# Kernel optimization log

Hardware: AMD Instinct MI355X
Metric: run time of the kernel (lower is better)

## Reference

```python
import jax, jax.numpy as jnp
import numpy as np

EPS = 1e-5
LAMB = 1.0
N_VARS = 40000
N_EDGES = 200000
N_CONF = 100000
FEAT = 128
DOM = 4
T_MAX = 3


def setup_inputs() -> dict:
    key = jax.random.key(0)
    ks = jax.random.split(key, 16)
    # initial node states: torch.rand then row-normalized (F.normalize dim=1)
    s = jax.random.uniform(ks[0], (N_VARS, FEAT), dtype=jnp.float32)
    state0 = s / jnp.maximum(jnp.linalg.norm(s, axis=1, keepdims=True), 1e-12)
    def lin(k, fan_in, shape):
        return jax.random.normal(k, shape, dtype=jnp.float32) / np.sqrt(fan_in)
    inp = {
        'state0': state0,
        'W1': lin(ks[1], 2 * FEAT, (2 * FEAT, FEAT)),
        'b1': jnp.zeros((FEAT,), jnp.float32),
        'W2': lin(ks[2], FEAT, (FEAT, FEAT)),
        'b2': jnp.zeros((FEAT,), jnp.float32),
        'ln_g': jnp.ones((FEAT,), jnp.float32),
        'ln_b': jnp.zeros((FEAT,), jnp.float32),
        'bn_g': jnp.ones((FEAT,), jnp.float32),
        'bn_b': jnp.zeros((FEAT,), jnp.float32),
        'Wd': lin(ks[3], FEAT, (FEAT, DOM)),
        'bd': jnp.zeros((DOM,), jnp.float32),
        # positive relation/confidence matrices so -log(...) is finite
        'relation': jax.random.uniform(ks[4], (DOM, DOM), jnp.float32, 0.1, 1.0),
        'confidence_mat': jax.random.uniform(ks[5], (DOM, DOM), jnp.float32, 0.1, 1.0),
        # positive degrees (divisor)
        'degrees': jax.random.uniform(ks[6], (N_VARS,), jnp.float32, 1.0, 33.0),
        'idx_left': jax.random.randint(ks[7], (N_EDGES,), 0, N_VARS, jnp.int32),
        'idx_right': jax.random.randint(ks[8], (N_EDGES,), 0, N_VARS, jnp.int32),
        'idx_left_pos': jax.random.randint(ks[9], (N_CONF,), 0, N_VARS, jnp.int32),
        'idx_right_pos': jax.random.randint(ks[10], (N_CONF,), 0, N_VARS, jnp.int32),
        'iterations': T_MAX,
    }
    return inp


def reference(state0, W1, b1, W2, b2, ln_g, ln_b, bn_g, bn_b, Wd, bd,
              relation, confidence_mat, degrees,
              idx_left, idx_right, idx_left_pos, idx_right_pos, iterations):
    N, F = state0.shape
    E = idx_left.shape[0]
    degs = degrees[:, None]

    def mlp(x):  # Linear-ReLU-Linear-ReLU-LayerNorm
        h = jax.nn.relu(x @ W1 + b1)
        h = jax.nn.relu(h @ W2 + b2)
        mu = jnp.mean(h, axis=-1, keepdims=True)
        var = jnp.var(h, axis=-1, keepdims=True)  # biased, like torch LayerNorm
        return ln_g * (h - mu) * jax.lax.rsqrt(var + EPS) + ln_b

    state = state0
    logits_list = []
    for _ in range(iterations):
        xl = state[idx_left]          # [E, F] gather
        xr = state[idx_right]
        # mpnn(in_right=xl, in_left=xr): in_lr = cat(xr, xl); in_rl = cat(xl, xr)
        msg = jnp.concatenate([jnp.concatenate([xr, xl], axis=1),
                               jnp.concatenate([xl, xr], axis=1)], axis=0)  # [2E, 2F]
        h = mlp(msg)
        agg = (jnp.zeros((N, F), state.dtype)
               .at[idx_left].add(h[:E])
               .at[idx_right].add(h[E:]))  # scatter-add messages
        rec = agg / degs
        # BatchNorm1d, training mode (batch stats over nodes)
        mu = jnp.mean(rec, axis=0)
        var = jnp.var(rec, axis=0)
        state = bn_g * (rec - mu) * jax.lax.rsqrt(var + EPS) + bn_b
        logits_list.append(state @ Wd + bd)

    phi = jax.nn.softmax(jnp.stack(logits_list, axis=1), axis=2)  # [N, T, D]
    T, D = phi.shape[1], phi.shape[2]
    all_phi = phi.reshape(N, T * D)

    def pair_loss(mat, il, ir, denom):
        pl = all_phi[il].reshape(-1, D)   # [E*T, D]
        pr = all_phi[ir].reshape(-1, D)
        s = jnp.sum((pl @ mat) * pr, axis=1)
        return jnp.sum(-jnp.log(s)) / denom

    n_conflicts = jnp.float32(E)
    n_confidence = jnp.float32(idx_left_pos.shape[0])
    loss = (pair_loss(relation, idx_left, idx_right, n_conflicts)
            + LAMB * pair_loss(confidence_mat, idx_left_pos, idx_right_pos, 10.0 * n_confidence))

    assignment = jnp.argmax(phi, axis=2).astype(jnp.int32)  # [N, T]
    valid = relation[assignment[idx_left], assignment[idx_right]]  # [E, T]
    edge_conflicts = 1.0 - valid
    n_conf = jnp.sum(edge_conflicts[:, -1])
    conflict_ratio = n_conf / n_conflicts
    return (loss, conflict_ratio, phi, edge_conflicts, assignment[:, -1], n_conf)
```

## Files before the change

### kernel.cpp

```cpp
#include <hip/hip_runtime.h>
#include <math.h>

#define N_VARS 40000
#define FEAT 128
#define N_EDGES 200000
#define N_MSG (2*N_EDGES)
#define N_CONFP 100000
#define T_ITERS 3
#define EPSF 1e-5f

#define NB_CONF 782
#define NB_PAIR 1172
#define NB_STAT 157
#define NB_STAT2 625
#define NB_MSG64 6250
#define OUT_TOTAL 1120003
#define NCONF_SLOT 1120002

typedef short short8 __attribute__((ext_vector_type(8)));
typedef float floatx4 __attribute__((ext_vector_type(4)));
typedef unsigned short ushort4v __attribute__((ext_vector_type(4)));
typedef unsigned uint4v __attribute__((ext_vector_type(4)));

__device__ __forceinline__ float scrub0(float x){
  unsigned u = __float_as_uint(x);
  return ((u & 0x7F800000u) == 0x7F800000u) ? 0.f : x;
}
__device__ __forceinline__ unsigned short f2bf_rne(float x){
  unsigned u = __float_as_uint(x);
  u += 0x7FFFu + ((u >> 16) & 1u);
  return (unsigned short)(u >> 16);
}
__device__ __forceinline__ float bf2f(unsigned short h){
  return __uint_as_float(((unsigned)h) << 16);
}
__device__ __forceinline__ unsigned cvtpk(float lo, float hi){
  unsigned r;
  asm("v_cvt_pk_bf16_f32 %0, %1, %2" : "=v"(r) : "v"(lo), "v"(hi));
  return r;
}

__global__ __launch_bounds__(256) void k_zero_int(int* __restrict__ p, int n){
  int i = blockIdx.x*256 + threadIdx.x;
  if (i < n) p[i] = 0;
}

__global__ __launch_bounds__(256) void k_hist(const int* __restrict__ idxL,
    const int* __restrict__ idxR, int* __restrict__ cnt){
  int m = blockIdx.x*256 + threadIdx.x;
  if (m < N_MSG){
    int t = (m < N_EDGES) ? idxL[m] : idxR[m - N_EDGES];
    atomicAdd(&cnt[t], 1);
  }
}
__global__ __launch_bounds__(256) void k_scan1(const int* __restrict__ cnt,
    int* __restrict__ pos, int* __restrict__ blk_tot){
  const int tid = threadIdx.x;
  const int idx = blockIdx.x*256 + tid;
  int v = (idx < N_VARS) ? cnt[idx] : 0;
  __shared__ int sh[256];
  sh[tid] = v;
  __syncthreads();
#pragma unroll
  for (int o = 1; o < 256; o <<= 1){
    int add = (tid >= o) ? sh[tid - o] : 0;
    __syncthreads();
    sh[tid] += add;
    __syncthreads();
  }
  if (idx < N_VARS) pos[idx] = sh[tid] - v;
  if (tid == 255) blk_tot[blockIdx.x] = sh[255];
}
__global__ __launch_bounds__(256) void k_scan2(const int* __restrict__ blk_tot,
    int* __restrict__ blk_off){
  const int tid = threadIdx.x;
  int v = (tid < NB_STAT) ? blk_tot[tid] : 0;
  __shared__ int sh[256];
  sh[tid] = v;
  __syncthreads();
#pragma unroll
  for (int o = 1; o < 256; o <<= 1){
    int add = (tid >= o) ? sh[tid - o] : 0;
    __syncthreads();
    sh[tid] += add;
    __syncthreads();
  }
  if (tid < NB_STAT) blk_off[tid] = sh[tid] - v;
}
__global__ __launch_bounds__(256) void k_scan3(int* __restrict__ pos,
    const int* __restrict__ blk_off){
  const int idx = blockIdx.x*256 + threadIdx.x;
  if (idx < N_VARS) pos[idx] += blk_off[blockIdx.x];
}
__global__ __launch_bounds__(256) void k_fill(const int* __restrict__ idxL,
    const int* __restrict__ idxR, int* __restrict__ pos,
    int2* __restrict__ pairs){
  int m = blockIdx.x*256 + threadIdx.x;
  if (m < N_MSG){
    int e = (m < N_EDGES) ? m : (m - N_EDGES);
    int l = idxL[e], r = idxR[e];
    int t = (m < N_EDGES) ? l : r;
    int o = (m < N_EDGES) ? r : l;
    int slot = atomicAdd(&pos[t], 1);
    pairs[slot] = make_int2(t, o);
  }
}

__global__ __launch_bounds__(256) void k_prep2(const float* __restrict__ W2,
                                               const float* __restrict__ W1,
                                               unsigned short* __restrict__ W2pack,
                                               unsigned short* __restrict__ W1pack){
  if (blockIdx.x < 8){
    int gid = blockIdx.x*256 + threadIdx.x;
    int lane = gid & 63;
    int ks = (gid >> 6) & 3;
    int ntg = gid >> 8;
    int kbase = ks*32 + (lane >> 4)*8;
    int n = ntg*16 + (lane & 15);
#pragma unroll
    for (int j = 0; j < 8; ++j)
      W2pack[gid*8 + j] = f2bf_rne(W2[(kbase + j)*FEAT + n]);
  } else {
    int gid = (blockIdx.x - 8)*256 + threadIdx.x;
    int lane = gid & 63;
    int ks = (gid >> 6) & 3;
    int ntg = gid >> 8;
    int kbase = ks*32 + (lane >> 4)*8;
    int n = ntg*16 + (lane & 15);
#pragma unroll
    for (int j = 0; j < 8; ++j){
      int k = kbase + j;
      float v = (n < 128) ? W1[k*FEAT + n] : W1[(128 + k)*FEAT + (n - 128)];
      W1pack[gid*8 + j] = f2bf_rne(v);
    }
  }
}

#define X_STRIDE 136
__global__ __launch_bounds__(256) void k_pq(const float* __restrict__ xf,
                                            const unsigned short* __restrict__ xb,
                                            int src_f32,
                                            const unsigned short* __restrict__ W1pack,
                                            const float* __restrict__ b1v,
                                            unsigned short* __restrict__ PQb,
                                            float* __restrict__ red,
                                            float4* __restrict__ recz){
  __shared__ __align__(16) unsigned short Xbf[32*X_STRIDE];
  const int tid = threadIdx.x;
  const int row0 = blockIdx.x * 32;
  if (blockIdx.x == 0) red[tid] = 0.f;
  {
    const int zid = blockIdx.x*256 + tid;
#pragma unroll
    for (int i = 0; i < 4; ++i)
      recz[zid + i*320000] = make_float4(0.f,0.f,0.f,0.f);
  }
  if (src_f32){
    const int c4 = (tid & 31)*4, g8 = tid >> 5;
#pragma unroll
    for (int r = 0; r < 4; ++r){
      int row = g8*4 + r;
      const float4 v = *(const float4*)&xf[(row0 + row)*FEAT + c4];
      uint2 uu;
      uu.x = cvtpk(v.x, v.y);
      uu.y = cvtpk(v.z, v.w);
      *(uint2*)&Xbf[row*X_STRIDE + c4] = uu;
    }
  } else {
    const int c8 = (tid & 15)*8, g16 = tid >> 4;
#pragma unroll
    for (int r = 0; r < 2; ++r){
      int row = r*16 + g16;
      *(short8*)&Xbf[row*X_STRIDE + c8] = *(const short8*)&xb[(row0 + row)*FEAT + c8];
    }
  }
  __syncthreads();
  const int w = tid >> 6, lane = tid & 63;
  const int quad = lane >> 4, mcol = lane & 15;
  float bi0 = 0.f, bi1 = 0.f, bi2 = 0.f, bi3 = 0.f;
  if (w >= 2){
    int nb = (w - 2)*64 + mcol;
    bi0 = b1v[nb]; bi1 = b1v[nb + 16]; bi2 = b1v[nb + 32]; bi3 = b1v[nb + 48];
  }
#pragma unroll
  for (int mt = 0; mt < 2; ++mt){
    floatx4 a0 = {bi0,bi0,bi0,bi0};
    floatx4 a1 = {bi1,bi1,bi1,bi1};
    floatx4 a2 = {bi2,bi2,bi2,bi2};
    floatx4 a3 = {bi3,bi3,bi3,bi3};
#pragma unroll
    for (int ks = 0; ks < 4; ++ks){
      short8 a = *(const short8*)&Xbf[(mt*16 + mcol)*X_STRIDE + ks*32 + quad*8];
      const unsigned short* bp = W1pack + ((w*16 + ks)*64 + lane)*8;
      short8 b0 = *(const short8*)(bp);
      short8 b1 = *(const short8*)(bp + 2048);
      short8 b2 = *(const short8*)(bp + 4096);
      short8 b3 = *(const short8*)(bp + 6144);
      a0 = __builtin_amdgcn_mfma_f32_16x16x32_bf16(a, b0, a0, 0, 0, 0);
      a1 = __builtin_amdgcn_mfma_f32_16x16x32_bf16(a, b1, a1, 0, 0, 0);
      a2 = __builtin_amdgcn_mfma_f32_16x16x32_bf16(a, b2, a2, 0, 0, 0);
      a3 = __builtin_amdgcn_mfma_f32_16x16x32_bf16(a, b3, a3, 0, 0, 0);
    }
#pragma unroll
    for (int reg = 0; reg < 4; ++reg){
      unsigned u01 = cvtpk(a0[reg], a1[reg]);
      unsigned u23 = cvtpk(a2[reg], a3[reg]);
      size_t base = (size_t)(row0 + mt*16 + quad*4 + reg)*(2*FEAT) + w*64 + mcol;
      PQb[base]      = (unsigned short)u01;
      PQb[base + 16] = (unsigned short)(u01 >> 16);
      PQb[base + 32] = (unsigned short)u23;
      PQb[base + 48] = (unsigned short)(u23 >> 16);
    }
  }
}

#define U_STRIDE 136
#define ZT_STRIDE 68

__global__ __launch_bounds__(256) void k_msgagg(const unsigned short* __restrict__ PQb,
    const unsigned short* __restrict__ W2pack,
    const float* __restrict__ b2v, const float* __restrict__ ln_g, const float* __restrict__ ln_b,
    const int2* __restrict__ pairs, const float* __restrict__ degrees,
    float* __restrict__ rec){
  __shared__ __align__(16) unsigned short Zbf[128*ZT_STRIDE];
  __shared__ int sTa[64];
  __shared__ float sDinv[64];
  __shared__ int sE[2];
  __shared__ unsigned sBrk[2];
  const int tid = threadIdx.x;
  const int s0 = blockIdx.x * 64;
  const int w = tid >> 6, lane = tid & 63;
  const int quad = lane >> 4, mcol = lane & 15;
  const int rbase = w*16;
  const int2 pr = pairs[s0 + rbase + mcol];
  const unsigned short* Prow = PQb + (size_t)pr.y*(2*FEAT) + quad*8;
  const unsigned short* Qrow = PQb + (size_t)pr.x*(2*FEAT) + FEAT + quad*8;
  short8 pch[4], qch[4];
#pragma unroll
  for (int ks = 0; ks < 4; ++ks){
    pch[ks] = *(const short8*)(Prow + ks*32);
    qch[ks] = *(const short8*)(Qrow + ks*32);
  }
  if (w == 0){
    int ta = pairs[s0 + lane].x;
    sTa[lane] = ta;
    sDinv[lane] = 1.f / degrees[ta];
    int tn = __shfl_down(ta, 1);
    bool d = (lane == 63) ? true : (tn != ta);
    unsigned long long b = __ballot(d);
    if (lane == 0){ sBrk[0] = (unsigned)b; sBrk[1] = (unsigned)(b >> 32); }
    if (lane == 62) sE[0] = (s0 == 0) ? -1 : pairs[s0 - 1].x;
    if (lane == 63) sE[1] = (s0 + 64 >= N_MSG) ? -1 : pairs[s0 + 64].x;
  }
  short8 afr[4];
#pragma unroll
  for (int ks = 0; ks < 4; ++ks){
    uint4v pu = *(const uint4v*)&pch[ks];
    uint4v qu = *(const uint4v*)&qch[ks];
    uint4v ou;
#pragma unroll
    for (int d = 0; d < 4; ++d){
      float plo = __uint_as_float(pu[d] << 16);
      float phi = __uint_as_float(pu[d] & 0xFFFF0000u);
      float qlo = __uint_as_float(qu[d] << 16);
      float qhi = __uint_as_float(qu[d] & 0xFFFF0000u);
      ou[d] = cvtpk(fmaxf(plo + qlo, 0.f), fmaxf(phi + qhi, 0.f));
    }
    afr[ks] = *(const short8*)&ou;
  }
  floatx4 acc[8];
#pragma unroll
  for (int nt = 0; nt < 8; ++nt){
    float b = b2v[nt*16 + mcol];
    acc[nt] = (floatx4){b, b, b, b};
  }
#pragma unroll
  for (int ks = 0; ks < 4; ++ks){
#pragma unroll
    for (int nt = 0; nt < 8; ++nt){
      short8 b = *(const short8*)(W2pack + ((nt*4 + ks)*64 + lane)*8);
      acc[nt] = __builtin_amdgcn_mfma_f32_16x16x32_bf16(afr[ks], b, acc[nt], 0, 0, 0);
    }
  }
  float z[8][4];
#pragma unroll
  for (int nt = 0; nt < 8; ++nt){
#pragma unroll
    for (int reg = 0; reg < 4; ++reg) z[nt][reg] = fmaxf(acc[nt][reg], 0.f);
  }
  float ps[4], pq[4];
#pragma unroll
  for (int reg = 0; reg < 4; ++reg){
    ps[reg] = 0.f; pq[reg] = 0.f;
#pragma unroll
    for (int nt = 0; nt < 8; ++nt){
      ps[reg] += z[nt][reg];
      pq[reg] += z[nt][reg]*z[nt][reg];
    }
  }
#pragma unroll
  for (int o = 1; o < 16; o <<= 1){
#pragma unroll
    for (int reg = 0; reg < 4; ++reg){
      ps[reg] += __shfl_xor(ps[reg], o);
      pq[reg] += __shfl_xor(pq[reg], o);
    }
  }
  float muv[4], rvv[4];
#pragma unroll
  for (int reg = 0; reg < 4; ++reg){
    float mu = ps[reg] * (1.f/FEAT);
    float var = fmaxf(pq[reg] * (1.f/FEAT) - mu*mu, 0.f);
    muv[reg] = mu;
    rvv[reg] = rsqrtf(var + EPSF);
  }
#pragma unroll
  for (int nt = 0; nt < 8; ++nt){
    float lg = ln_g[nt*16 + mcol];
    float lb = ln_b[nt*16 + mcol];
    float o0 = scrub0(lg*(z[nt][0] - muv[0])*rvv[0] + lb);
    float o1 = scrub0(lg*(z[nt][1] - muv[1])*rvv[1] + lb);
    float o2 = scrub0(lg*(z[nt][2] - muv[2])*rvv[2] + lb);
    float o3 = scrub0(lg*(z[nt][3] - muv[3])*rvv[3] + lb);
    uint2 u; u.x = cvtpk(o0, o1); u.y = cvtpk(o2, o3);
    *(uint2*)&Zbf[(nt*16 + mcol)*ZT_STRIDE + rbase + quad*4] = u;
  }
  __syncthreads();
  {
    const int col = tid & 127, h = tid >> 7;
    const int rbeg = h*32;
    const unsigned bm = __builtin_amdgcn_readfirstlane(sBrk[h]);
    ushort4v rv4[8];
#pragma unroll
    for (int k = 0; k < 8; ++k)
      rv4[k] = *(const ushort4v*)&Zbf[col*ZT_STRIDE + rbeg + k*4];
    float accv = 0.f;
    int cur = sTa[rbeg];
    bool part = (rbeg == 0) ? (sE[0] == cur) : (sTa[rbeg-1] == cur);
#pragma unroll
    for (int i = 0; i < 32; ++i){
      accv += bf2f((unsigned short)rv4[i >> 2][i & 3]);
      const bool realbrk = (bm >> i) & 1u;
      if ((i == 31) | realbrk){
        const int r = rbeg + i;
        bool cont = (i == 31) && ((r == 63) ? (sE[1] == cur) : !realbrk);
        float v = accv * sDinv[r];
        float* dst = &rec[(size_t)cur*FEAT + col];
        if (part | cont) atomicAdd(dst, v);
        else *dst = v;
        accv = 0.f;
        part = false;
        if (i < 31) cur = sTa[r + 1];
      }
    }
  }
}

__global__ __launch_bounds__(256) void k_edge(const unsigned short* __restrict__ PQb,
    const unsigned short* __restrict__ W2pack,
    const float* __restrict__ b2v, const float* __restrict__ ln_g, const float* __restrict__ ln_b,
    const int* __restrict__ idxL, const int* __restrict__ idxR,
    float* __restrict__ agg){
  __shared__ __align__(16) unsigned short Ubf[32*U_STRIDE];
  __shared__ float sS[64], sQ[64];
  __shared__ int sTa[32], sTb[32];
  const int tid = threadIdx.x;
  const int m0 = blockIdx.x * 32;
  if (tid < 32){
    int m = m0 + tid;
    int e = (m < N_EDGES) ? m : (m - N_EDGES);
    int l = idxL[e], r = idxR[e];
    sTa[tid] = (m < N_EDGES) ? l : r;
    sTb[tid] = (m < N_EDGES) ? r : l;
  }
  __syncthreads();
  {
    const int c8 = (tid & 15)*8, g16 = tid >> 4;
#pragma unroll
    for (int r = 0; r < 2; ++r){
      int row = r*16 + g16;
      short8 pb = *(const short8*)&PQb[sTb[row]*(2*FEAT) + c8];
      short8 qb = *(const short8*)&PQb[sTa[row]*(2*FEAT) + FEAT + c8];
      float f[8];
#pragma unroll
      for (int j = 0; j < 8; ++j)
        f[j] = fmaxf(bf2f((unsigned short)pb[j]) + bf2f((unsigned short)qb[j]), 0.f);
      uint4 uu;
      uu.x = cvtpk(f[0], f[1]);
      uu.y = cvtpk(f[2], f[3]);
      uu.z = cvtpk(f[4], f[5]);
      uu.w = cvtpk(f[6], f[7]);
      *(uint4*)&Ubf[row*U_STRIDE + c8] = uu;
    }
  }
  __syncthreads();
  const int w = tid >> 6, lane = tid & 63;
  const int mt = w & 1, nhalf = w >> 1;
  const int quad = lane >> 4, mcol = lane & 15;
  float bb0 = b2v[nhalf*64 + 0*16 + mcol];
  float bb1 = b2v[nhalf*64 + 1*16 + mcol];
  float bb2 = b2v[nhalf*64 + 2*16 + mcol];
  float bb3 = b2v[nhalf*64 + 3*16 + mcol];
  floatx4 acc0 = {bb0,bb0,bb0,bb0};
  floatx4 acc1 = {bb1,bb1,bb1,bb1};
  floatx4 acc2 = {bb2,bb2,bb2,bb2};
  floatx4 acc3 = {bb3,bb3,bb3,bb3};
#pragma unroll
  for (int ks = 0; ks < 4; ++ks){
    short8 a = *(const short8*)&Ubf[(mt*16 + mcol)*U_STRIDE + ks*32 + quad*8];
    const unsigned short* bp = W2pack + ((nhalf*4*256) + ks*64 + lane)*8;
    short8 bq0 = *(const short8*)(bp);
    short8 bq1 = *(const short8*)(bp + 2048);
    short8 bq2 = *(const short8*)(bp + 4096);
    short8 bq3 = *(const short8*)(bp + 6144);
    acc0 = __builtin_amdgcn_mfma_f32_16x16x32_bf16(a, bq0, acc0, 0, 0, 0);
    acc1 = __builtin_amdgcn_mfma_f32_16x16x32_bf16(a, bq1, acc1, 0, 0, 0);
    acc2 = __builtin_amdgcn_mfma_f32_16x16x32_bf16(a, bq2, acc2, 0, 0, 0);
    acc3 = __builtin_amdgcn_mfma_f32_16x16x32_bf16(a, bq3, acc3, 0, 0, 0);
  }
  float z[4][4];
#pragma unroll
  for (int nt = 0; nt < 4; ++nt){
    floatx4 a4 = (nt == 0) ? acc0 : (nt == 1) ? acc1 : (nt == 2) ? acc2 : acc3;
#pragma unroll
    for (int reg = 0; reg < 4; ++reg) z[nt][reg] = fmaxf(a4[reg], 0.f);
  }
  float ps[4], pq[4];
#pragma unroll
  for (int reg = 0; reg < 4; ++reg){
    ps[reg] = z[0][reg] + z[1][reg] + z[2][reg] + z[3][reg];
    pq[reg] = z[0][reg]*z[0][reg] + z[1][reg]*z[1][reg] + z[2][reg]*z[2][reg] + z[3][reg]*z[3][reg];
  }
#pragma unroll
  for (int o = 1; o < 16; o <<= 1){
#pragma unroll
    for (int reg = 0; reg < 4; ++reg){
      ps[reg] += __shfl_xor(ps[reg], o);
      pq[reg] += __shfl_xor(pq[reg], o);
    }
  }
  if (mcol == 0){
#pragma unroll
    for (int reg = 0; reg < 4; ++reg){
      int row = mt*16 + quad*4 + reg;
      sS[nhalf*32 + row] = ps[reg];
      sQ[nhalf*32 + row] = pq[reg];
    }
  }
  __syncthreads();
  int colv[4]; float lgv[4], lbv[4];
#pragma unroll
  for (int nt = 0; nt < 4; ++nt){
    colv[nt] = nhalf*64 + nt*16 + mcol;
    lgv[nt] = ln_g[colv[nt]];
    lbv[nt] = ln_b[colv[nt]];
  }
#pragma unroll
  for (int reg = 0; reg < 4; ++reg){
    int row = mt*16 + quad*4 + reg;
    float s = sS[row] + sS[32 + row];
    float q = sQ[row] + sQ[32 + row];
    float mu = s * (1.f/FEAT);
    float var = fmaxf(q * (1.f/FEAT) - mu*mu, 0.f);
    float rv = rsqrtf(var + EPSF);
    int a = sTa[row];
#pragma unroll
    for (int nt = 0; nt < 4; ++nt){
      float o = scrub0(lgv[nt]*(z[nt][reg] - mu)*rv + lbv[nt]);
      atomicAdd(&agg[a*FEAT + colv[nt]], o);
    }
  }
}

__global__ __launch_bounds__(256) void k_stats(const float* __restrict__ src,
    const float* __restrict__ degrees, int divide, float* __restrict__ red){
  const int tid = threadIdx.x;
  const int j = tid & 127, half_sel = tid >> 7;
  const int n0 = blockIdx.x * 64;
  float s1 = 0.f, s2 = 0.f;
  for (int i = half_sel; i < 64; i += 2){
    int n = n0 + i;
    float v = src[n*FEAT + j];
    if (divide) v /= degrees[n];
    s1 += v;
    s2 += v*v;
  }
  __shared__ float sh1[256], sh2[256];
  sh1[tid] = s1; sh2[tid] = s2;
  __syncthreads();
  if (half_sel == 0){
    atomicAdd(&red[j],       sh1[tid] + sh1[tid+128]);
    atomicAdd(&red[128 + j], sh2[tid] + sh2[tid+128]);
  }
}

__global__ __launch_bounds__(256) void k_bn(const float* __restrict__ src,
    const float* __restrict__ degrees, int divide, const float* __restrict__ red,
    const float* __restrict__ bn_g, const float* __restrict__ bn_b,
    const float* __restrict__ Wd, const float* __restrict__ bd,
    unsigned short* __restrict__ state_bf, int* __restrict__ asg,
    float* __restrict__ out_phi, float* __restrict__ out_asg, int t){
  const int w = threadIdx.x >> 6, l = threadIdx.x & 63;
  const int n = blockIdx.x*4 + w;
  const float invN = 1.f / (float)N_VARS;
  float mu0 = red[l]*invN,     mu1 = red[l+64]*invN;
  float v0  = fmaxf(red[128+l]*invN    - mu0*mu0, 0.f);
  float v1  = fmaxf(red[128+l+64]*invN - mu1*mu1, 0.f);
  float rv0 = rsqrtf(v0 + EPSF);
  float rv1 = rsqrtf(v1 + EPSF);
  float dinv = divide ? (1.f / degrees[n]) : 1.f;
  float r0 = src[n*FEAT + l]    * dinv;
  float r1 = src[n*FEAT + l+64] * dinv;
  float s0 = scrub0(bn_g[l]   *(r0 - mu0)*rv0 + bn_b[l]);
  float s1 = scrub0(bn_g[l+64]*(r1 - mu1)*rv1 + bn_b[l+64]);
  state_bf[n*FEAT + l]    = f2bf_rne(s0);
  state_bf[n*FEAT + l+64] = f2bf_rne(s1);
  float p[4];
#pragma unroll
  for (int d = 0; d < 4; ++d)
    p[d] = s0*Wd[l*4 + d] + s1*Wd[(l+64)*4 + d];
#pragma unroll
  for (int o = 32; o > 0; o >>= 1){
#pragma unroll
    for (int d = 0; d < 4; ++d) p[d] += __shfl_xor(p[d], o);
  }
  if (l == 0){
    float lg[4];
#pragma unroll
    for (int d = 0; d < 4; ++d) lg[d] = scrub0(p[d] + bd[d]);
    float mx = fmaxf(fmaxf(lg[0],lg[1]), fmaxf(lg[2],lg[3]));
    float ex[4]; float ssum = 0.f;
#pragma unroll
    for (int d = 0; d < 4; ++d){ ex[d] = expf(lg[d] - mx); ssum += ex[d]; }
    float inv = 1.f / ssum;
    int am = 0; float bv = -1.f;
#pragma unroll
    for (int d = 0; d < 4; ++d){
      float pv = scrub0(ex[d]*inv);
      out_phi[n*12 + t*4 + d] = pv;
      if (pv > bv){ bv = pv; am = d; }
    }
    asg[n*3 + t] = am;
    if (t == 2) out_asg[n] = (float)am;
  }
}

__global__ __launch_bounds__(256) void k_lossconf(const float* __restrict__ phi,
    const int* __restrict__ iL, const int* __restrict__ iR,
    const int* __restrict__ iLp, const int* __restrict__ iRp,
    const float* __restrict__ rel, const float* __restrict__ conf,
    const int* __restrict__ asg, float* __restrict__ out_ec,
    float* __restrict__ part_l1, float* __restrict__ part_l2,
    float* __restrict__ part_conf){
  if (blockIdx.x < NB_PAIR){
    const int e = blockIdx.x*256 + threadIdx.x;
    float p1 = 0.f, p2 = 0.f;
    if (e < N_EDGES + N_CONFP){
      const int isrel = (e < N_EDGES);
      const int l = isrel ? iL[e] : iLp[e - N_EDGES];
      const int r = isrel ? iR[e] : iRp[e - N_EDGES];
      const float* M = isrel ? rel : conf;
      const float2* plp = (const float2*)(phi + (size_t)l*12);
      const float2* prp = (const float2*)(phi + (size_t)r*12);
      float L[12], R[12];
#pragma unroll
      for (int k = 0; k < 6; ++k){
        float2 a = plp[k], b = prp[k];
        L[2*k] = a.x; L[2*k+1] = a.y;
        R[2*k] = b.x; R[2*k+1] = b.y;
      }
      float acc = 0.f;
#pragma unroll
      for (int tt = 0; tt < 3; ++tt){
        const float* a = L + tt*4;
        const float* b = R + tt*4;
        float s = 0.f;
#pragma unroll
        for (int j = 0; j < 4; ++j){
          float tj = a[0]*M[0*4+j] + a[1]*M[1*4+j] + a[2]*M[2*4+j] + a[3]*M[3*4+j];
          s += tj*b[j];
        }
        s = scrub0(s); s = fmaxf(s, 1e-35f);
        acc -= __logf(s);
      }
      if (isrel) p1 = acc; else p2 = acc;
    }
    __shared__ float sh1[256], sh2[256];
    sh1[threadIdx.x] = p1; sh2[threadIdx.x] = p2;
    __syncthreads();
    for (int k = 128; k > 0; k >>= 1){
      if (threadIdx.x < k){
        sh1[threadIdx.x] += sh1[threadIdx.x + k];
        sh2[threadIdx.x] += sh2[threadIdx.x + k];
      }
      __syncthreads();
    }
    if (threadIdx.x == 0){
      part_l1[blockIdx.x] = sh1[0];
      part_l2[blockIdx.x] = sh2[0];
    }
  } else {
    const int bid = blockIdx.x - NB_PAIR;
    const int e = bid*256 + threadIdx.x;
    float c2 = 0.f;
    if (e < N_EDGES){
      int l = iL[e], r = iR[e];
#pragma unroll
      for (int tt = 0; tt < 3; ++tt){
        int ai = asg[l*3+tt] & 3, bi = asg[r*3+tt] & 3;
        float c = scrub0(1.f - rel[ai*4 + bi]);
        out_ec[e*3 + tt] = c;
        if (tt == 2) c2 = c;
      }
    }
    __shared__ float sh[256];
    sh[threadIdx.x] = c2;
    __syncthreads();
    for (int k = 128; k > 0; k >>= 1){
      if (threadIdx.x < k) sh[threadIdx.x] += sh[threadIdx.x + k];
      __syncthreads();
    }
    if (threadIdx.x == 0) part_conf[bid] = sh[0];
  }
}

__global__ __launch_bounds__(256) void k_fin(const float* __restrict__ part_conf,
    const float* __restrict__ part_l1, const float* __restrict__ part_l2,
    float* __restrict__ out){
  const int tid = threadIdx.x;
  float a = 0.f, ca = 0.f, b = 0.f, cb = 0.f, c = 0.f;
  for (int i = tid; i < NB_PAIR; i += 256){
    float y = part_l1[i] - ca; float t = a + y; ca = (t - a) - y; a = t;
    float y2 = part_l2[i] - cb; float t2 = b + y2; cb = (t2 - b) - y2; b = t2;
  }
  for (int i = tid; i < NB_CONF; i += 256) c += part_conf[i];
  __shared__ float sh1[256], sh2[256], sh3[256];
  sh1[tid] = a; sh2[tid] = b; sh3[tid] = c;
  __syncthreads();
  for (int k = 128; k > 0; k >>= 1){
    if (tid < k){
      sh1[tid] += sh1[tid + k];
      sh2[tid] += sh2[tid + k];
      sh3[tid] += sh3[tid + k];
    }
    __syncthreads();
  }
  if (tid == 0){
    out[0] = sh1[0]/(float)N_EDGES + sh2[0]/(10.f*(float)N_CONFP);
    float nc = sh3[0];
    out[NCONF_SLOT] = nc;
    out[1] = nc / (float)N_EDGES;
  }
}

extern "C" void kernel_launch(void* const* d_in, const int* in_sizes, int n_in,
                              void* d_out, int out_size, void* d_ws, size_t ws_size,
                              hipStream_t stream){
  const float* state0  = (const float*)d_in[0];
  const float* W1      = (const float*)d_in[1];
  const float* b1v     = (const float*)d_in[2];
  const float* W2      = (const float*)d_in[3];
  const float* b2v     = (const float*)d_in[4];
  const float* ln_g    = (const float*)d_in[5];
  const float* ln_b    = (const float*)d_in[6];
  const float* bn_g    = (const float*)d_in[7];
  const float* bn_b    = (const float*)d_in[8];
  const float* Wd      = (const float*)d_in[9];
  const float* bd      = (const float*)d_in[10];
  const float* rel     = (const float*)d_in[11];
  const float* confm   = (const float*)d_in[12];
  const float* degrees = (const float*)d_in[13];
  const int* idxL = (const int*)d_in[14];
  const int* idxR = (const int*)d_in[15];
  const int* iLp  = (const int*)d_in[16];
  const int* iRp  = (const int*)d_in[17];

  char* ws = (char*)d_ws;
  unsigned short* state_bf = (unsigned short*)(ws);
  unsigned short* PQb  = (unsigned short*)(ws + 10240000);
  float*  recagg    = (float*)(ws + 30720000);
  int*    asg       = (int*)  (ws + 51200000);
  float*  red       = (float*)(ws + 51840768);
  float*  part_l1   = (float*)(ws + 51841792);
  float*  part_l2   = (float*)(ws + 51855860);
  float*  part_conf = (float*)(ws + 51869928);
  unsigned short* W2pack = (unsigned short*)(ws + 51873056);
  unsigned short* W1pack = (unsigned short*)(ws + 51905824);
  int*    pos       = (int*)(ws + 51971360);
  int*    cnt       = (int*)(ws + 52131360);
  int2*   pairs     = (int2*)(ws + 52291360);
  int*    blk_tot   = (int*)(ws + 55491360);
  int*    blk_off   = (int*)(ws + 55492384);
  const int use_csr = (ws_size >= (size_t)55493408) ? 1 : 0;

  float* out     = (float*)d_out;
  float* out_phi = out + 2;
  float* out_ec  = out + 480002;
  float* out_asg = out + 1080002;

  k_prep2<<<24, 256, 0, stream>>>(W2, W1, W2pack, W1pack);

  if (use_csr){
    k_zero_int<<<NB_STAT, 256, 0, stream>>>(cnt, N_VARS);
    k_hist<<<(N_MSG + 255)/256, 256, 0, stream>>>(idxL, idxR, cnt);
    k_scan1<<<NB_STAT, 256, 0, stream>>>(cnt, pos, blk_tot);
    k_scan2<<<1, 256, 0, stream>>>(blk_tot, blk_off);
    k_scan3<<<NB_STAT, 256, 0, stream>>>(pos, blk_off);
    k_fill<<<(N_MSG + 255)/256, 256, 0, stream>>>(idxL, idxR, pos, pairs);
  }

  for (int t = 0; t < T_ITERS; ++t){
    k_pq<<<N_VARS/32, 256, 0, stream>>>(state0, state_bf, (t == 0) ? 1 : 0, W1pack, b1v,
                                        PQb, red, (float4*)recagg);
    if (use_csr){
      k_msgagg<<<NB_MSG64, 256, 0, stream>>>(PQb, W2pack, b2v, ln_g, ln_b,
                                             pairs, degrees, recagg);
      k_stats<<<NB_STAT2, 256, 0, stream>>>(recagg, degrees, 0, red);
      k_bn<<<N_VARS/4, 256, 0, stream>>>(recagg, degrees, 0, red, bn_g, bn_b, Wd, bd,
                                         state_bf, asg, out_phi, out_asg, t);
    } else {
      k_edge<<<N_MSG/32, 256, 0, stream>>>(PQb, W2pack, b2v, ln_g, ln_b, idxL, idxR, recagg);
      k_stats<<<NB_STAT2, 256, 0, stream>>>(recagg, degrees, 1, red);
      k_bn<<<N_VARS/4, 256, 0, stream>>>(recagg, degrees, 1, red, bn_g, bn_b, Wd, bd,
                                         state_bf, asg, out_phi, out_asg, t);
    }
  }
  k_lossconf<<<NB_PAIR + NB_CONF, 256, 0, stream>>>(out_phi, idxL, idxR, iLp, iRp, rel, confm,
                                                    asg, out_ec, part_l1, part_l2, part_conf);
  k_fin<<<1, 256, 0, stream>>>(part_conf, part_l1, part_l2, out);
}
```

Baseline: 536.8 us.

## Stage P rows and deduplicated per-run Q rows in LDS for message aggregation

The msgagg kernel now loads the P rows for each message cooperatively into LDS with coalesced 16-byte loads. Because messages are sorted by target, Q rows are fetched only once per distinct target run rather than once per message, and each row finds its Q row through a popcount-derived run id. Every wave now computes the break ballot itself, which removes the sBrk shared slots. LDS use grows, since two 64x136 bf16 buffers are reused for the Z transpose, and an extra __syncthreads is added before that reuse. This may lower occupancy.

```diff
diff --git a/kernel.cpp b/kernel.cpp
--- a/kernel.cpp
+++ b/kernel.cpp
@@ -222,41 +222,59 @@
     const float* __restrict__ b2v, const float* __restrict__ ln_g, const float* __restrict__ ln_b,
     const int2* __restrict__ pairs, const float* __restrict__ degrees,
     float* __restrict__ rec){
-  __shared__ __align__(16) unsigned short Zbf[128*ZT_STRIDE];
+  __shared__ __align__(16) unsigned short PZ[64*U_STRIDE];
+  __shared__ __align__(16) unsigned short Qlds[64*U_STRIDE];
+  __shared__ int sTrun[64];
   __shared__ int sTa[64];
   __shared__ float sDinv[64];
   __shared__ int sE[2];
-  __shared__ unsigned sBrk[2];
   const int tid = threadIdx.x;
   const int s0 = blockIdx.x * 64;
   const int w = tid >> 6, lane = tid & 63;
+  const int ta = pairs[s0 + lane].x;
+  const int tn = __shfl_down(ta, 1);
+  const bool brk = (lane == 63) ? true : (tn != ta);
+  const unsigned long long bm = __ballot(brk);
+  const int nruns = __popcll(bm);
+  const bool isstart = (lane == 0) || ((bm >> (lane - 1)) & 1ull);
+  const int ridlane = (int)__popcll(bm & ((1ull << lane) - 1ull));
+  if (isstart) sTrun[ridlane] = ta;
+  if (w == 0){
+    sTa[lane] = ta;
+    sDinv[lane] = 1.f / degrees[ta];
+    if (lane == 62) sE[0] = (s0 == 0) ? -1 : pairs[s0 - 1].x;
+    if (lane == 63) sE[1] = (s0 + 64 >= N_MSG) ? -1 : pairs[s0 + 64].x;
+  }
+  const int c8 = (tid & 15)*8, g16 = tid >> 4;
+#pragma unroll
+  for (int r = 0; r < 4; ++r){
+    int row = r*16 + g16;
+    int other = pairs[s0 + row].y;
+    *(short8*)&PZ[row*U_STRIDE + c8] =
+        *(const short8*)&PQb[(size_t)other*(2*FEAT) + c8];
+  }
+  asm volatile("s_waitcnt lgkmcnt(0)" ::: "memory");
+  {
+    const int q4 = lane >> 4;
+    const int c8l = (lane & 15)*8;
+    for (int k = w*4 + q4; k < nruns; k += 16){
+      int tgt = sTrun[k];
+      *(short8*)&Qlds[k*U_STRIDE + c8l] =
+          *(const short8*)&PQb[(size_t)tgt*(2*FEAT) + FEAT + c8l];
+    }
+  }
+  __syncthreads();
   const int quad = lane >> 4, mcol = lane & 15;
   const int rbase = w*16;
-  const int2 pr = pairs[s0 + rbase + mcol];
-  const unsigned short* Prow = PQb + (size_t)pr.y*(2*FEAT) + quad*8;
-  const unsigned short* Qrow = PQb + (size_t)pr.x*(2*FEAT) + FEAT + quad*8;
-  short8 pch[4], qch[4];
+  const int myrow = rbase + mcol;
+  const int myrid = (int)__popcll(bm & ((1ull << myrow) - 1ull));
+  short8 afr[4];
 #pragma unroll
   for (int ks = 0; ks < 4; ++ks){
-    pch[ks] = *(const short8*)(Prow + ks*32);
-    qch[ks] = *(const short8*)(Qrow + ks*32);
-  }
-  if (w == 0){
-    int ta = pairs[s0 + lane].x;
-    sTa[lane] = ta;
-    sDinv[lane] = 1.f / degrees[ta];
-    int tn = __shfl_down(ta, 1);
-    bool d = (lane == 63) ? true : (tn != ta);
-    unsigned long long b = __ballot(d);
-    if (lane == 0){ sBrk[0] = (unsigned)b; sBrk[1] = (unsigned)(b >> 32); }
-    if (lane == 62) sE[0] = (s0 == 0) ? -1 : pairs[s0 - 1].x;
-    if (lane == 63) sE[1] = (s0 + 64 >= N_MSG) ? -1 : pairs[s0 + 64].x;
-  }
-  short8 afr[4];
-#pragma unroll
-  for (int ks = 0; ks < 4; ++ks){
-    uint4v pu = *(const uint4v*)&pch[ks];
-    uint4v qu = *(const uint4v*)&qch[ks];
+    short8 pc = *(const short8*)&PZ[myrow*U_STRIDE + ks*32 + quad*8];
+    short8 qc = *(const short8*)&Qlds[myrid*U_STRIDE + ks*32 + quad*8];
+    uint4v pu = *(const uint4v*)&pc;
+    uint4v qu = *(const uint4v*)&qc;
     uint4v ou;
 #pragma unroll
     for (int d = 0; d < 4; ++d){
@@ -314,6 +332,7 @@
     muv[reg] = mu;
     rvv[reg] = rsqrtf(var + EPSF);
   }
+  unsigned w0p[8], w1p[8];
 #pragma unroll
   for (int nt = 0; nt < 8; ++nt){
     float lg = ln_g[nt*16 + mcol];
@@ -322,25 +341,31 @@
     float o1 = scrub0(lg*(z[nt][1] - muv[1])*rvv[1] + lb);
     float o2 = scrub0(lg*(z[nt][2] - muv[2])*rvv[2] + lb);
     float o3 = scrub0(lg*(z[nt][3] - muv[3])*rvv[3] + lb);
-    uint2 u; u.x = cvtpk(o0, o1); u.y = cvtpk(o2, o3);
-    *(uint2*)&Zbf[(nt*16 + mcol)*ZT_STRIDE + rbase + quad*4] = u;
+    w0p[nt] = cvtpk(o0, o1);
+    w1p[nt] = cvtpk(o2, o3);
+  }
+  __syncthreads();
+#pragma unroll
+  for (int nt = 0; nt < 8; ++nt){
+    uint2 u; u.x = w0p[nt]; u.y = w1p[nt];
+    *(uint2*)&PZ[(nt*16 + mcol)*ZT_STRIDE + rbase + quad*4] = u;
   }
   __syncthreads();
   {
     const int col = tid & 127, h = tid >> 7;
     const int rbeg = h*32;
-    const unsigned bm = __builtin_amdgcn_readfirstlane(sBrk[h]);
+    const unsigned bmh = (unsigned)(h ? (bm >> 32) : bm);
     ushort4v rv4[8];
 #pragma unroll
     for (int k = 0; k < 8; ++k)
-      rv4[k] = *(const ushort4v*)&Zbf[col*ZT_STRIDE + rbeg + k*4];
+      rv4[k] = *(const ushort4v*)&PZ[col*ZT_STRIDE + rbeg + k*4];
     float accv = 0.f;
     int cur = sTa[rbeg];
     bool part = (rbeg == 0) ? (sE[0] == cur) : (sTa[rbeg-1] == cur);
 #pragma unroll
     for (int i = 0; i < 32; ++i){
       accv += bf2f((unsigned short)rv4[i >> 2][i & 3]);
-      const bool realbrk = (bm >> i) & 1u;
+      const bool realbrk = (bmh >> i) & 1u;
       if ((i == 31) | realbrk){
         const int r = rbeg + i;
         bool cont = (i == 31) && ((r == 63) ? (sE[1] == cur) : !realbrk);
```

Result: slower. 561.1 us (+4.5%).
